# Performance work log

Measured on AMD Instinct MI355X. Metric: run time of the kernel, lower is better.

The kernel has to match this reference:

```python
import jax, jax.numpy as jnp
import numpy as np

N_IN, N_OUT, C_IN, C_OUT = 60000, 160000, 128, 128
EPS = 1e-3          # BN eps from norm_cfg dict(type='BN1d', eps=0.001)
SLOPE = 0.01        # nn.LeakyReLU default negative_slope


def _sparse_conv(feat, W, idx_in, idx_out, n_out):
    """Gather-GEMM-scatter sparse conv: for each kernel offset k,
    out[idx_out[k]] += feat[idx_in[k]] @ W[k]. Loop is over the small fixed
    kernel-tap count (9 or 27), never over voxels."""
    out = jnp.zeros((n_out, W.shape[2]), feat.dtype)
    for k in range(W.shape[0]):
        out = out.at[idx_out[k]].add(feat[idx_in[k]] @ W[k])
    return out


def _lrelu(x):
    return jnp.where(x > 0, x, SLOPE * x)


def _bn(f, g, b):
    # BatchNorm1d in training mode: batch stats over active voxels (axis 0)
    m = f.mean(axis=0)
    v = f.var(axis=0)
    return (f - m) * jax.lax.rsqrt(v + EPS) * g + b


def setup_inputs() -> dict:
    key = jax.random.key(0)
    ks = jax.random.split(key, 16)

    def w(k, K, ci, co):
        return jax.random.normal(k, (K, ci, co), jnp.float32) * (1.0 / np.sqrt(K * ci))

    def idx(k, K, P, hi):
        return jax.random.randint(k, (K, P), 0, hi, dtype=jnp.int32)

    ones = jnp.ones((C_OUT,), jnp.float32)
    zeros = jnp.zeros((C_OUT,), jnp.float32)
    return {
        "x_feat": jax.random.normal(ks[0], (N_IN, C_IN), jnp.float32),
        "skip_feat": jax.random.normal(ks[1], (N_OUT, C_OUT), jnp.float32),
        "W_t": w(ks[2], 27, C_IN, C_OUT), "g_t": ones, "b_t": zeros,
        "W_up": w(ks[3], 27, C_OUT, C_OUT),
        "W1": w(ks[4], 9, C_OUT, C_OUT), "g1": ones, "b1": zeros,
        "W2": w(ks[5], 9, C_OUT, C_OUT), "g2": ones, "b2": zeros,
        "W3": w(ks[6], 27, C_OUT, C_OUT), "g3": ones, "b3": zeros,
        "ti_in": idx(ks[7], 27, N_IN, N_IN),
        "ti_out": idx(ks[8], 27, N_IN, N_IN),
        "ui_in": idx(ks[9], 27, N_OUT, N_IN),
        "ui_out": idx(ks[10], 27, N_OUT, N_OUT),
        "i1_in": idx(ks[11], 9, N_OUT, N_OUT),
        "i1_out": idx(ks[12], 9, N_OUT, N_OUT),
        "i2_in": idx(ks[13], 9, N_OUT, N_OUT),
        "i2_out": idx(ks[14], 9, N_OUT, N_OUT),
        "i3_in": idx(ks[15], 27, N_OUT, N_OUT),
        "i3_out": idx(jax.random.fold_in(key, 99), 27, N_OUT, N_OUT),
    }


def reference(x_feat, skip_feat, W_t, g_t, b_t, W_up,
              W1, g1, b1, W2, g2, b2, W3, g3, b3,
              ti_in, ti_out, ui_in, ui_out,
              i1_in, i1_out, i2_in, i2_out, i3_in, i3_out):
    n_in = x_feat.shape[0]
    n_out = skip_feat.shape[0]
    # trans_dilao (3x3x3 subm) -> LeakyReLU -> BN
    upA = _bn(_lrelu(_sparse_conv(x_feat, W_t, ti_in, ti_out, n_in)), g_t, b_t)
    # SparseInverseConv3d (upsample to skip voxel set) + residual add
    upA = _sparse_conv(upA, W_up, ui_in, ui_out, n_out) + skip_feat
    # conv1 (1,3,3) -> act -> bn
    upE = _bn(_lrelu(_sparse_conv(upA, W1, i1_in, i1_out, n_out)), g1, b1)
    # conv2 (3,1,3) -> act -> bn
    upE = _bn(_lrelu(_sparse_conv(upE, W2, i2_in, i2_out, n_out)), g2, b2)
    # conv3 (3,3,3) -> act -> bn
    upE = _bn(_lrelu(_sparse_conv(upE, W3, i3_in, i3_out, n_out)), g3, b3)
    return upE
```

## Files before the change

kernel.cpp:

```cpp
#include <hip/hip_runtime.h>
#include <hip/hip_bf16.h>

typedef __attribute__((ext_vector_type(8))) short bf16x8;
typedef __attribute__((ext_vector_type(4))) short short4v;
typedef __attribute__((ext_vector_type(2))) _Float16 half2v;
typedef __attribute__((ext_vector_type(4))) _Float16 half4v;
typedef __attribute__((ext_vector_type(4))) float f32x4;

#define N_IN  60000
#define N_OUT 160000
#define C     128
#define EPS   1e-3f
#define SLOPE 0.01f

__device__ inline short f2bf(float f) {
    unsigned u = __builtin_bit_cast(unsigned, f);
    u += 0x7FFFu + ((u >> 16) & 1u);
    return (short)(u >> 16);
}
__device__ inline float bf2f(short s) {
    unsigned u = ((unsigned)(unsigned short)s) << 16;
    return __builtin_bit_cast(float, u);
}
__device__ inline float lrelu(float x) { return x > 0.f ? x : SLOPE * x; }

__device__ inline void pk_atomic_add_f16(_Float16* addr, float lo, float hi) {
    half2v v; v.x = (_Float16)lo; v.y = (_Float16)hi;
#if __has_builtin(__builtin_amdgcn_global_atomic_fadd_v2f16)
    __builtin_amdgcn_global_atomic_fadd_v2f16((half2v*)addr, v);
#else
    unsigned pk = __builtin_bit_cast(unsigned, v);
    asm volatile("global_atomic_pk_add_f16 %0, %1, off" :: "v"(addr), "v"(pk) : "memory");
#endif
}

__global__ __launch_bounds__(256) void k_f32_to_bf16(const float* __restrict__ in,
                                                     short* __restrict__ out, int count4) {
    int i = blockIdx.x * 256 + threadIdx.x, stride = gridDim.x * 256;
    for (; i < count4; i += stride) {
        f32x4 v = ((const f32x4*)in)[i];
        short4v o;
        o.x = f2bf(v.x); o.y = f2bf(v.y); o.z = f2bf(v.z); o.w = f2bf(v.w);
        ((short4v*)out)[i] = o;
    }
}

__global__ __launch_bounds__(256) void k_f32_to_f16(const float* __restrict__ in,
                                                    _Float16* __restrict__ out, int count4) {
    int i = blockIdx.x * 256 + threadIdx.x, stride = gridDim.x * 256;
    for (; i < count4; i += stride) {
        f32x4 v = ((const f32x4*)in)[i];
        half4v o;
        o.x = (_Float16)v.x; o.y = (_Float16)v.y; o.z = (_Float16)v.z; o.w = (_Float16)v.w;
        ((half4v*)out)[i] = o;
    }
}

__global__ __launch_bounds__(256) void k_f16_to_bf16(const _Float16* __restrict__ in,
                                                     short* __restrict__ out, int count4) {
    int i = blockIdx.x * 256 + threadIdx.x, stride = gridDim.x * 256;
    for (; i < count4; i += stride) {
        half4v v = ((const half4v*)in)[i];
        short4v o;
        o.x = f2bf((float)v.x); o.y = f2bf((float)v.y);
        o.z = f2bf((float)v.z); o.w = f2bf((float)v.w);
        ((short4v*)out)[i] = o;
    }
}

__global__ __launch_bounds__(256) void k_conv(const short* __restrict__ feat,
                                              const float* __restrict__ W,
                                              const int* __restrict__ idx_in,
                                              const int* __restrict__ idx_out,
                                              _Float16* __restrict__ out,
                                              int P, int ntiles) {
    const int k    = blockIdx.y;
    const int lane = threadIdx.x & 63;
    const int wave = threadIdx.x >> 6;
    const int l15  = lane & 15, lhi = lane >> 4;
    const int wcol0 = wave * 32;

    const float* Wk = W + (size_t)k * C * C;
    const int* iin  = idx_in  + (size_t)k * P;
    const int* iout = idx_out + (size_t)k * P;

    bf16x8 bfr[2][4];
#pragma unroll
    for (int n = 0; n < 2; n++)
#pragma unroll
        for (int kk = 0; kk < 4; kk++) {
            const int co = wcol0 + 16 * n + l15;
            const int k0 = kk * 32 + lhi * 8;
            bf16x8 b;
#pragma unroll
            for (int j = 0; j < 8; j++) b[j] = f2bf(Wk[(size_t)(k0 + j) * C + co]);
            bfr[n][kk] = b;
        }

    int t = blockIdx.x;
    if (t >= ntiles) return;
    const int stride = gridDim.x;

    int ix[4]; int4 io[4];
#pragma unroll
    for (int m = 0; m < 4; m++) {
        int pa = t * 64 + 16 * m + l15;
        ix[m] = (pa < P) ? iin[pa] : -1;
        int pb = t * 64 + 16 * m + lhi * 4;
        io[m] = (pb < P) ? *(const int4*)(iout + pb) : make_int4(0, 0, 0, 0);
    }
    bf16x8 afr[4][4];
#pragma unroll
    for (int m = 0; m < 4; m++) {
        if (ix[m] >= 0) {
            const bf16x8* rp = (const bf16x8*)(feat + (size_t)ix[m] * C);
#pragma unroll
            for (int kk = 0; kk < 4; kk++) afr[m][kk] = rp[kk * 4 + lhi];
        } else {
#pragma unroll
            for (int kk = 0; kk < 4; kk++) {
                bf16x8 z;
#pragma unroll
                for (int j = 0; j < 8; j++) z[j] = 0;
                afr[m][kk] = z;
            }
        }
    }
    {
        int tn = t + stride;
#pragma unroll
        for (int m = 0; m < 4; m++) {
            int pa = tn * 64 + 16 * m + l15;
            ix[m] = (tn < ntiles && pa < P) ? iin[pa] : -1;
        }
    }

    const f32x4 zero4 = {0.f, 0.f, 0.f, 0.f};
    while (t < ntiles) {
        const int tn = t + stride;
        f32x4 acc[4][2];
#pragma unroll
        for (int m = 0; m < 4; m++) { acc[m][0] = zero4; acc[m][1] = zero4; }
#pragma unroll
        for (int m = 0; m < 4; m++)
#pragma unroll
            for (int kk = 0; kk < 4; kk++) {
                acc[m][0] = __builtin_amdgcn_mfma_f32_16x16x32_bf16(afr[m][kk], bfr[0][kk], acc[m][0], 0, 0, 0);
                acc[m][1] = __builtin_amdgcn_mfma_f32_16x16x32_bf16(afr[m][kk], bfr[1][kk], acc[m][1], 0, 0, 0);
            }

        int4 ioN[4];
#pragma unroll
        for (int m = 0; m < 4; m++) {
            int pb = tn * 64 + 16 * m + lhi * 4;
            ioN[m] = (tn < ntiles && pb < P) ? *(const int4*)(iout + pb) : make_int4(0, 0, 0, 0);
        }
#pragma unroll
        for (int m = 0; m < 4; m++) {
            if (ix[m] >= 0) {
                const bf16x8* rp = (const bf16x8*)(feat + (size_t)ix[m] * C);
#pragma unroll
                for (int kk = 0; kk < 4; kk++) afr[m][kk] = rp[kk * 4 + lhi];
            } else {
#pragma unroll
                for (int kk = 0; kk < 4; kk++) {
                    bf16x8 z;
#pragma unroll
                    for (int j = 0; j < 8; j++) z[j] = 0;
                    afr[m][kk] = z;
                }
            }
        }
        {
            int t2 = tn + stride;
#pragma unroll
            for (int m = 0; m < 4; m++) {
                int pa = t2 * 64 + 16 * m + l15;
                ix[m] = (t2 < ntiles && pa < P) ? iin[pa] : -1;
            }
        }

#pragma unroll
        for (int m = 0; m < 4; m++) {
            const int pbase = t * 64 + 16 * m + lhi * 4;
            const int4 ro = io[m];
#pragma unroll
            for (int r = 0; r < 4; r++) {
                float v0 = acc[m][0][r], v1 = acc[m][1][r];
                float x0 = __shfl_xor(v0, 1, 64);
                float x1 = __shfl_xor(v1, 1, 64);
                if (pbase < P) {
                    int col; float lo, hi;
                    if ((l15 & 1) == 0) { lo = v0; hi = x0; col = wcol0 + l15; }
                    else                { lo = x1; hi = v1; col = wcol0 + 15 + l15; }
                    const int orow = (&ro.x)[r];
                    pk_atomic_add_f16(out + (size_t)orow * C + col, lo, hi);
                }
            }
        }
#pragma unroll
        for (int m = 0; m < 4; m++) io[m] = ioN[m];
        t = tn;
    }
}

__global__ __launch_bounds__(256) void k_stats(const _Float16* __restrict__ x, int n,
                                               float* __restrict__ stats) {
    const int t  = threadIdx.x;
    const int c4 = (t & 31) * 4;
    const int rg = t >> 5;
    float s0 = 0, s1 = 0, s2 = 0, s3 = 0, q0 = 0, q1 = 0, q2 = 0, q3 = 0;
    for (int r = blockIdx.x * 8 + rg; r < n; r += gridDim.x * 8) {
        half4v v = *(const half4v*)(x + (size_t)r * C + c4);
        float y0 = lrelu((float)v.x), y1 = lrelu((float)v.y);
        float y2 = lrelu((float)v.z), y3 = lrelu((float)v.w);
        s0 += y0; s1 += y1; s2 += y2; s3 += y3;
        q0 += y0 * y0; q1 += y1 * y1; q2 += y2 * y2; q3 += y3 * y3;
    }
    __shared__ float rs[8][128];
    __shared__ float rq[8][128];
    rs[rg][c4] = s0; rs[rg][c4 + 1] = s1; rs[rg][c4 + 2] = s2; rs[rg][c4 + 3] = s3;
    rq[rg][c4] = q0; rq[rg][c4 + 1] = q1; rq[rg][c4 + 2] = q2; rq[rg][c4 + 3] = q3;
    __syncthreads();
    if (t < 128) {
        float S = 0, Q = 0;
#pragma unroll
        for (int g = 0; g < 8; g++) { S += rs[g][t]; Q += rq[g][t]; }
        unsafeAtomicAdd(&stats[t], S);
        unsafeAtomicAdd(&stats[128 + t], Q);
    }
}

__global__ __launch_bounds__(256) void k_apply(const _Float16* x, const float* __restrict__ stats,
                                               const float* __restrict__ g, const float* __restrict__ b,
                                               int n, float inv_n,
                                               short* __restrict__ out_bf, float* out_f) {
    __shared__ float sc[128], sh[128];
    const int t = threadIdx.x;
    if (t < 128) {
        float m = stats[t] * inv_n;
        float v = stats[128 + t] * inv_n - m * m;
        float s = rsqrtf(v + EPS) * g[t];
        sc[t] = s; sh[t] = b[t] - m * s;
    }
    __syncthreads();
    const int c4 = (t & 31) * 4;
    const int rg = t >> 5;
    const float s0 = sc[c4], s1 = sc[c4 + 1], s2 = sc[c4 + 2], s3 = sc[c4 + 3];
    const float h0 = sh[c4], h1 = sh[c4 + 1], h2 = sh[c4 + 2], h3 = sh[c4 + 3];
    for (int r = blockIdx.x * 8 + rg; r < n; r += gridDim.x * 8) {
        half4v v = *(const half4v*)(x + (size_t)r * C + c4);
        f32x4 o;
        o.x = lrelu((float)v.x) * s0 + h0;
        o.y = lrelu((float)v.y) * s1 + h1;
        o.z = lrelu((float)v.z) * s2 + h2;
        o.w = lrelu((float)v.w) * s3 + h3;
        if (out_f) *(f32x4*)(out_f + (size_t)r * C + c4) = o;
        if (out_bf) {
            short4v ob;
            ob.x = f2bf(o.x); ob.y = f2bf(o.y); ob.z = f2bf(o.z); ob.w = f2bf(o.w);
            *(short4v*)(out_bf + (size_t)r * C + c4) = ob;
        }
    }
}

extern "C" void kernel_launch(void* const* d_in, const int* in_sizes, int n_in,
                              void* d_out, int out_size, void* d_ws, size_t ws_size,
                              hipStream_t stream) {
    const float* x_feat = (const float*)d_in[0];
    const float* skip   = (const float*)d_in[1];
    const float* W_t  = (const float*)d_in[2];
    const float* g_t  = (const float*)d_in[3];
    const float* b_t  = (const float*)d_in[4];
    const float* W_up = (const float*)d_in[5];
    const float* W1   = (const float*)d_in[6];
    const float* g1   = (const float*)d_in[7];
    const float* b1   = (const float*)d_in[8];
    const float* W2   = (const float*)d_in[9];
    const float* g2   = (const float*)d_in[10];
    const float* b2   = (const float*)d_in[11];
    const float* W3   = (const float*)d_in[12];
    const float* g3   = (const float*)d_in[13];
    const float* b3   = (const float*)d_in[14];
    const int* ti_in  = (const int*)d_in[15];
    const int* ti_out = (const int*)d_in[16];
    const int* ui_in  = (const int*)d_in[17];
    const int* ui_out = (const int*)d_in[18];
    const int* i1_in  = (const int*)d_in[19];
    const int* i1_out = (const int*)d_in[20];
    const int* i2_in  = (const int*)d_in[21];
    const int* i2_out = (const int*)d_in[22];
    const int* i3_in  = (const int*)d_in[23];
    const int* i3_out = (const int*)d_in[24];

    char*     ws    = (char*)d_ws;
    short*    A     = (short*)ws;
    short*    B     = (short*)(ws + 40960000);
    _Float16* Bh    = (_Float16*)B;
    float*    stats = (float*)(ws + 81920000);
    _Float16* H     = (_Float16*)d_out;
    float*    outF  = (float*)d_out;

    k_f32_to_bf16<<<1024, 256, 0, stream>>>(x_feat, A, N_IN * C / 4);
    hipMemsetAsync(H, 0, (size_t)N_IN * C * 2, stream);
    k_conv<<<dim3(80, 27), 256, 0, stream>>>(A, W_t, ti_in, ti_out, H, N_IN, (N_IN + 63) / 64);
    hipMemsetAsync(stats, 0, 1024, stream);
    k_stats<<<512, 256, 0, stream>>>(H, N_IN, stats);
    k_apply<<<512, 256, 0, stream>>>(H, stats, g_t, b_t, N_IN, 1.f / N_IN, B, nullptr);

    k_f32_to_f16<<<2048, 256, 0, stream>>>(skip, H, N_OUT * C / 4);
    k_conv<<<dim3(80, 27), 256, 0, stream>>>(B, W_up, ui_in, ui_out, H, N_OUT, N_OUT / 64);
    k_f16_to_bf16<<<2048, 256, 0, stream>>>(H, A, N_OUT * C / 4);

    hipMemsetAsync(H, 0, (size_t)N_OUT * C * 2, stream);
    k_conv<<<dim3(240, 9), 256, 0, stream>>>(A, W1, i1_in, i1_out, H, N_OUT, N_OUT / 64);
    hipMemsetAsync(stats, 0, 1024, stream);
    k_stats<<<512, 256, 0, stream>>>(H, N_OUT, stats);
    k_apply<<<512, 256, 0, stream>>>(H, stats, g1, b1, N_OUT, 1.f / N_OUT, B, nullptr);

    hipMemsetAsync(H, 0, (size_t)N_OUT * C * 2, stream);
    k_conv<<<dim3(240, 9), 256, 0, stream>>>(B, W2, i2_in, i2_out, H, N_OUT, N_OUT / 64);
    hipMemsetAsync(stats, 0, 1024, stream);
    k_stats<<<512, 256, 0, stream>>>(H, N_OUT, stats);
    k_apply<<<512, 256, 0, stream>>>(H, stats, g2, b2, N_OUT, 1.f / N_OUT, A, nullptr);

    hipMemsetAsync(Bh, 0, (size_t)N_OUT * C * 2, stream);
    k_conv<<<dim3(80, 27), 256, 0, stream>>>(A, W3, i3_in, i3_out, Bh, N_OUT, N_OUT / 64);
    hipMemsetAsync(stats, 0, 1024, stream);
    k_stats<<<512, 256, 0, stream>>>(Bh, N_OUT, stats);
    k_apply<<<512, 256, 0, stream>>>(Bh, stats, g3, b3, N_OUT, 1.f / N_OUT, nullptr, outF);
}
```

Before: 3.070 ms.

## Stage conv outputs through LDS so each wave atomically adds contiguous rows

The gather-GEMM-scatter conv kernel now writes its packed f16 accumulator pairs into a padded LDS tile instead of issuing atomics straight from the MFMA fragment layout. After a barrier, each wave issues packed f16 atomics for 16 output rows, and the 64 lanes of each atomic cover one full 256-byte row, so the scatter is coalesced rather than spread across rows. Output indices are loaded once per lane and broadcast with shuffles. This adds two block barriers per tile and LDS traffic in exchange for fewer scattered atomic transactions.

```diff
diff --git a/kernel.cpp b/kernel.cpp
--- a/kernel.cpp
+++ b/kernel.cpp
@@ -12,24 +12,23 @@
 #define C     128
 #define EPS   1e-3f
 #define SLOPE 0.01f
+#define LDSW  65
 
 __device__ inline short f2bf(float f) {
     unsigned u = __builtin_bit_cast(unsigned, f);
     u += 0x7FFFu + ((u >> 16) & 1u);
     return (short)(u >> 16);
 }
-__device__ inline float bf2f(short s) {
-    unsigned u = ((unsigned)(unsigned short)s) << 16;
-    return __builtin_bit_cast(float, u);
-}
 __device__ inline float lrelu(float x) { return x > 0.f ? x : SLOPE * x; }
 
-__device__ inline void pk_atomic_add_f16(_Float16* addr, float lo, float hi) {
+__device__ inline unsigned pack_f16(float lo, float hi) {
     half2v v; v.x = (_Float16)lo; v.y = (_Float16)hi;
+    return __builtin_bit_cast(unsigned, v);
+}
+__device__ inline void pk_atomic_add_raw(_Float16* addr, unsigned pk) {
 #if __has_builtin(__builtin_amdgcn_global_atomic_fadd_v2f16)
-    __builtin_amdgcn_global_atomic_fadd_v2f16((half2v*)addr, v);
+    __builtin_amdgcn_global_atomic_fadd_v2f16((half2v*)addr, __builtin_bit_cast(half2v, pk));
 #else
-    unsigned pk = __builtin_bit_cast(unsigned, v);
     asm volatile("global_atomic_pk_add_f16 %0, %1, off" :: "v"(addr), "v"(pk) : "memory");
 #endif
 }
@@ -74,6 +73,8 @@
                                               const int* __restrict__ idx_out,
                                               _Float16* __restrict__ out,
                                               int P, int ntiles) {
+    __shared__ unsigned lds_t[64 * LDSW];
+
     const int k    = blockIdx.y;
     const int lane = threadIdx.x & 63;
     const int wave = threadIdx.x >> 6;
@@ -100,14 +101,13 @@
     int t = blockIdx.x;
     if (t >= ntiles) return;
     const int stride = gridDim.x;
-
-    int ix[4]; int4 io[4];
+    const int dwcol = (wcol0 >> 1) + ((l15 & 1) ? 8 + (l15 >> 1) : (l15 >> 1));
+
+    int ix[4];
 #pragma unroll
     for (int m = 0; m < 4; m++) {
         int pa = t * 64 + 16 * m + l15;
         ix[m] = (pa < P) ? iin[pa] : -1;
-        int pb = t * 64 + 16 * m + lhi * 4;
-        io[m] = (pb < P) ? *(const int4*)(iout + pb) : make_int4(0, 0, 0, 0);
     }
     bf16x8 afr[4][4];
 #pragma unroll
@@ -125,6 +125,11 @@
                 afr[m][kk] = z;
             }
         }
+    }
+    int io_cur;
+    {
+        int p = t * 64 + wave * 16 + lane;
+        io_cur = (lane < 16 && p < P) ? iout[p] : 0;
     }
     {
         int tn = t + stride;
@@ -149,11 +154,10 @@
                 acc[m][1] = __builtin_amdgcn_mfma_f32_16x16x32_bf16(afr[m][kk], bfr[1][kk], acc[m][1], 0, 0, 0);
             }
 
-        int4 ioN[4];
-#pragma unroll
-        for (int m = 0; m < 4; m++) {
-            int pb = tn * 64 + 16 * m + lhi * 4;
-            ioN[m] = (tn < ntiles && pb < P) ? *(const int4*)(iout + pb) : make_int4(0, 0, 0, 0);
+        int ioN;
+        {
+            int p = tn * 64 + wave * 16 + lane;
+            ioN = (tn < ntiles && lane < 16 && p < P) ? iout[p] : 0;
         }
 #pragma unroll
         for (int m = 0; m < 4; m++) {
@@ -181,25 +185,28 @@
         }
 
 #pragma unroll
-        for (int m = 0; m < 4; m++) {
-            const int pbase = t * 64 + 16 * m + lhi * 4;
-            const int4 ro = io[m];
+        for (int m = 0; m < 4; m++)
 #pragma unroll
             for (int r = 0; r < 4; r++) {
                 float v0 = acc[m][0][r], v1 = acc[m][1][r];
                 float x0 = __shfl_xor(v0, 1, 64);
                 float x1 = __shfl_xor(v1, 1, 64);
-                if (pbase < P) {
-                    int col; float lo, hi;
-                    if ((l15 & 1) == 0) { lo = v0; hi = x0; col = wcol0 + l15; }
-                    else                { lo = x1; hi = v1; col = wcol0 + 15 + l15; }
-                    const int orow = (&ro.x)[r];
-                    pk_atomic_add_f16(out + (size_t)orow * C + col, lo, hi);
-                }
-            }
-        }
-#pragma unroll
-        for (int m = 0; m < 4; m++) io[m] = ioN[m];
+                unsigned pk = ((l15 & 1) == 0) ? pack_f16(v0, x0) : pack_f16(x1, v1);
+                int prow = 16 * m + lhi * 4 + r;
+                lds_t[prow * LDSW + dwcol] = pk;
+            }
+        __syncthreads();
+
+#pragma unroll
+        for (int row = 0; row < 16; row++) {
+            unsigned v = lds_t[(wave * 16 + row) * LDSW + lane];
+            int orow = __shfl(io_cur, row, 64);
+            if (t * 64 + wave * 16 + row < P)
+                pk_atomic_add_raw(out + (size_t)orow * C + 2 * lane, v);
+        }
+        __syncthreads();
+
+        io_cur = ioN;
         t = tn;
     }
 }
```

Measured after the change: 3.155 ms. +2.7%, slower.
